# Kernel optimization log

Hardware: AMD Instinct MI355X
Metric: run time of the kernel (lower is better)

The kernel has to match this reference:

```python
import jax, jax.numpy as jnp
import numpy as np

HIDDEN = 4096
INTER = 11008
GROUP = 128
B, S = 1, 2048


def setup_inputs() -> dict:
    key = jax.random.key(0)
    ks = jax.random.split(key, 10)
    inp = {
        "x": jax.random.normal(ks[0], (B, S, HIDDEN), dtype=jnp.float32),
        "gate_qw": jax.random.randint(ks[1], (INTER, HIDDEN), 0, 16, dtype=jnp.int32),
        "gate_qz": jax.random.randint(ks[2], (INTER, HIDDEN // GROUP), 0, 16, dtype=jnp.int32),
        "gate_scale": jax.random.uniform(ks[3], (INTER, HIDDEN // GROUP), dtype=jnp.float32) * 0.02,
        "gate_bias": jnp.zeros((INTER,), dtype=jnp.float32),
        "up_qw": jax.random.randint(ks[4], (INTER, HIDDEN), 0, 16, dtype=jnp.int32),
        "up_qz": jax.random.randint(ks[5], (INTER, HIDDEN // GROUP), 0, 16, dtype=jnp.int32),
        "up_scale": jax.random.uniform(ks[6], (INTER, HIDDEN // GROUP), dtype=jnp.float32) * 0.02,
        "up_bias": jnp.zeros((INTER,), dtype=jnp.float32),
        "down_qw": jax.random.randint(ks[7], (HIDDEN, INTER), 0, 16, dtype=jnp.int32),
        "down_qz": jax.random.randint(ks[8], (HIDDEN, INTER // GROUP), 0, 16, dtype=jnp.int32),
        "down_scale": jax.random.uniform(ks[9], (HIDDEN, INTER // GROUP), dtype=jnp.float32) * 0.02,
        "down_bias": jnp.zeros((HIDDEN,), dtype=jnp.float32),
        "group_size": GROUP,
    }
    return inp


def _dequant(qw, qz, scale, group_size):
    # qw: [O, I] int codes in [0,16); qz, scale: [O, I//g]
    O, I = qw.shape
    g = group_size
    q = qw.reshape(O, I // g, g).astype(jnp.float32)
    w = (q - qz[:, :, None].astype(jnp.float32)) * scale[:, :, None]
    return w.reshape(O, I)  # [O, I]


def reference(x, gate_qw, gate_qz, gate_scale, gate_bias,
              up_qw, up_qz, up_scale, up_bias,
              down_qw, down_qz, down_scale, down_bias, group_size):
    Wg = _dequant(gate_qw, gate_qz, gate_scale, group_size)   # [INTER, HIDDEN]
    Wu = _dequant(up_qw, up_qz, up_scale, group_size)         # [INTER, HIDDEN]
    Wd = _dequant(down_qw, down_qz, down_scale, group_size)   # [HIDDEN, INTER]
    g = jnp.einsum('bsh,ih->bsi', x, Wg) + gate_bias          # [B,S,INTER]
    u = jnp.einsum('bsh,ih->bsi', x, Wu) + up_bias            # [B,S,INTER]
    h = jax.nn.silu(g) * u                                    # SwiGLU
    y = jnp.einsum('bsi,hi->bsh', h, Wd) + down_bias          # [B,S,HIDDEN]
    return y
```

## Files before the change

kernel.cpp:

```cpp
#include <hip/hip_runtime.h>
#include <hip/hip_bf16.h>
#include <stdint.h>

#define SEQ    2048
#define HIDDEN 4096
#define INTER  11008

typedef short bf16x8 __attribute__((ext_vector_type(8)));
typedef float f32x4  __attribute__((ext_vector_type(4)));
typedef unsigned short u16x8 __attribute__((ext_vector_type(8)));

__device__ __forceinline__ unsigned short f2bf(float f) {
    union { __hip_bfloat16 h; unsigned short u; } v;
    v.h = __float2bfloat16(f);
    return v.u;
}

__device__ __forceinline__ void gload_lds16(const void* g, void* lds) {
    __builtin_amdgcn_global_load_lds(
        (const __attribute__((address_space(1))) uint32_t*)g,
        (__attribute__((address_space(3))) uint32_t*)lds,
        16, 0, 0);
}

__device__ __forceinline__ void deq_block(
    const int* __restrict__ qw, const int* __restrict__ qz,
    const float* __restrict__ sc, unsigned short* __restrict__ w,
    int db, int t)
{
    size_t i = (size_t)db * 4096 + (size_t)t * 8;
    int gi = (int)(i >> 7);
    int   z = qz[gi];
    float s = sc[gi];
    float zs = -(float)z * s;
    int4 q0 = *(const int4*)(qw + i);
    int4 q1 = *(const int4*)(qw + i + 4);
    u16x8 o;
    o[0] = f2bf(fmaf((float)q0.x, s, zs));
    o[1] = f2bf(fmaf((float)q0.y, s, zs));
    o[2] = f2bf(fmaf((float)q0.z, s, zs));
    o[3] = f2bf(fmaf((float)q0.w, s, zs));
    o[4] = f2bf(fmaf((float)q1.x, s, zs));
    o[5] = f2bf(fmaf((float)q1.y, s, zs));
    o[6] = f2bf(fmaf((float)q1.z, s, zs));
    o[7] = f2bf(fmaf((float)q1.w, s, zs));
    *(u16x8*)(w + i) = o;
}

__global__ __launch_bounds__(512) void k_prep(
    const float* __restrict__ x, unsigned short* __restrict__ xb,
    const int* __restrict__ gqw, const int* __restrict__ gqz,
    const float* __restrict__ gsc, unsigned short* __restrict__ wgb,
    const int* __restrict__ uqw, const int* __restrict__ uqz,
    const float* __restrict__ usc, unsigned short* __restrict__ wub)
{
    const int bid = blockIdx.x;
    const int t   = threadIdx.x;
    if (bid < 2048) {
        size_t i = ((size_t)bid * 512 + t) * 8;
        float4 v0 = *(const float4*)(x + i);
        float4 v1 = *(const float4*)(x + i + 4);
        u16x8 o;
        o[0] = f2bf(v0.x); o[1] = f2bf(v0.y); o[2] = f2bf(v0.z); o[3] = f2bf(v0.w);
        o[4] = f2bf(v1.x); o[5] = f2bf(v1.y); o[6] = f2bf(v1.z); o[7] = f2bf(v1.w);
        *(u16x8*)(xb + i) = o;
    } else if (bid < 13056) {
        deq_block(gqw, gqz, gsc, wgb, bid - 2048, t);
    } else {
        deq_block(uqw, uqz, usc, wub, bid - 13056, t);
    }
}

__global__ __launch_bounds__(512) void k_deq_fb(
    const int* __restrict__ qw, const int* __restrict__ qz,
    const float* __restrict__ sc, unsigned short* __restrict__ w)
{
    deq_block(qw, qz, sc, w, blockIdx.x, threadIdx.x);
}

__global__ __launch_bounds__(512) void k_gate_up(
    const unsigned short* __restrict__ xb,
    const unsigned short* __restrict__ wg,
    const unsigned short* __restrict__ wu,
    const float* __restrict__ gbias, const float* __restrict__ ubias,
    unsigned short* __restrict__ h,
    const int* __restrict__ dqw, const int* __restrict__ dqz,
    const float* __restrict__ dsc, unsigned short* __restrict__ wdb)
{
    __shared__ __align__(16) unsigned short At[128 * 64];
    __shared__ __align__(16) unsigned short Bg[128 * 64];
    __shared__ __align__(16) unsigned short Bu[128 * 64];

    if (blockIdx.x >= 1376) {
        deq_block(dqw, dqz, dsc, wdb, blockIdx.x - 1376, threadIdx.x);
        return;
    }

    const int orig = blockIdx.x;
    const int swz  = (orig & 7) * 172 + (orig >> 3);
    const int mt   = swz & 15;
    const int nt   = swz >> 4;
    const int m0   = mt * 128;
    const int n0   = nt * 128;

    const int t    = threadIdx.x;
    const int lane = t & 63;
    const int wave = t >> 6;
    const int wm = (wave >> 2) * 64;
    const int wn = (wave & 3) * 32;

    f32x4 accG[4][2], accU[4][2];
#pragma unroll
    for (int mi = 0; mi < 4; ++mi)
#pragma unroll
        for (int ni = 0; ni < 2; ++ni) {
            accG[mi][ni] = (f32x4){0.f, 0.f, 0.f, 0.f};
            accU[mi][ni] = (f32x4){0.f, 0.f, 0.f, 0.f};
        }

    for (int kt = 0; kt < HIDDEN / 64; ++kt) {
        const int k0 = kt * 64;

#pragma unroll
        for (int cc = 0; cc < 2; ++cc) {
            int idx  = t + 512 * cc;
            int row  = idx >> 3;
            int scol = ((idx & 7) * 16) ^ ((row & 7) << 4);
            gload_lds16((const char*)(xb + (size_t)(m0 + row) * HIDDEN + k0) + scol,
                        (char*)At + idx * 16);
            gload_lds16((const char*)(wg + (size_t)(n0 + row) * HIDDEN + k0) + scol,
                        (char*)Bg + idx * 16);
            gload_lds16((const char*)(wu + (size_t)(n0 + row) * HIDDEN + k0) + scol,
                        (char*)Bu + idx * 16);
        }

        __syncthreads();

#pragma unroll
        for (int kk = 0; kk < 2; ++kk) {
            bf16x8 af[4], bg[2], bu[2];
#pragma unroll
            for (int mi = 0; mi < 4; ++mi) {
                int row  = wm + mi * 16 + (lane & 15);
                int colb = kk * 64 + ((lane >> 4) * 16);
                af[mi] = *(const bf16x8*)((const char*)At + row * 128 +
                                          (colb ^ ((row & 7) << 4)));
            }
#pragma unroll
            for (int ni = 0; ni < 2; ++ni) {
                int row  = wn + ni * 16 + (lane & 15);
                int colb = kk * 64 + ((lane >> 4) * 16);
                int off  = row * 128 + (colb ^ ((row & 7) << 4));
                bg[ni] = *(const bf16x8*)((const char*)Bg + off);
                bu[ni] = *(const bf16x8*)((const char*)Bu + off);
            }
            __builtin_amdgcn_s_setprio(1);
#pragma unroll
            for (int mi = 0; mi < 4; ++mi)
#pragma unroll
                for (int ni = 0; ni < 2; ++ni) {
                    accG[mi][ni] = __builtin_amdgcn_mfma_f32_16x16x32_bf16(
                        af[mi], bg[ni], accG[mi][ni], 0, 0, 0);
                    accU[mi][ni] = __builtin_amdgcn_mfma_f32_16x16x32_bf16(
                        af[mi], bu[ni], accU[mi][ni], 0, 0, 0);
                }
            __builtin_amdgcn_s_setprio(0);
        }

        __syncthreads();
    }

#pragma unroll
    for (int ni = 0; ni < 2; ++ni) {
        int col = n0 + wn + ni * 16 + (lane & 15);
        float gb = gbias[col], ub = ubias[col];
#pragma unroll
        for (int mi = 0; mi < 4; ++mi) {
#pragma unroll
            for (int j = 0; j < 4; ++j) {
                int row = m0 + wm + mi * 16 + ((lane >> 4) * 4) + j;
                float g = accG[mi][ni][j] + gb;
                float u = accU[mi][ni][j] + ub;
                float sig = 1.f / (1.f + __expf(-g));
                h[(size_t)row * INTER + col] = f2bf(g * sig * u);
            }
        }
    }
}

__global__ __launch_bounds__(512) void k_down(
    const unsigned short* __restrict__ h,
    const unsigned short* __restrict__ wd,
    const float* __restrict__ dbias,
    float* __restrict__ y)
{
    __shared__ __align__(16) unsigned short At[128 * 64];
    __shared__ __align__(16) unsigned short Bd[128 * 64];

    const int orig = blockIdx.x;
    const int swz  = (orig & 7) * 64 + (orig >> 3);
    const int mt   = swz & 15;
    const int nt   = swz >> 4;
    const int m0   = mt * 128;
    const int n0   = nt * 128;

    const int t    = threadIdx.x;
    const int lane = t & 63;
    const int wave = t >> 6;
    const int wm = (wave >> 2) * 64;
    const int wn = (wave & 3) * 32;

    f32x4 acc[4][2];
#pragma unroll
    for (int mi = 0; mi < 4; ++mi)
#pragma unroll
        for (int ni = 0; ni < 2; ++ni)
            acc[mi][ni] = (f32x4){0.f, 0.f, 0.f, 0.f};

    for (int kt = 0; kt < INTER / 64; ++kt) {
        const int k0 = kt * 64;

#pragma unroll
        for (int cc = 0; cc < 2; ++cc) {
            int idx  = t + 512 * cc;
            int row  = idx >> 3;
            int scol = ((idx & 7) * 16) ^ ((row & 7) << 4);
            gload_lds16((const char*)(h + (size_t)(m0 + row) * INTER + k0) + scol,
                        (char*)At + idx * 16);
            gload_lds16((const char*)(wd + (size_t)(n0 + row) * INTER + k0) + scol,
                        (char*)Bd + idx * 16);
        }

        __syncthreads();

#pragma unroll
        for (int kk = 0; kk < 2; ++kk) {
            bf16x8 af[4], bd[2];
#pragma unroll
            for (int mi = 0; mi < 4; ++mi) {
                int row  = wm + mi * 16 + (lane & 15);
                int colb = kk * 64 + ((lane >> 4) * 16);
                af[mi] = *(const bf16x8*)((const char*)At + row * 128 +
                                          (colb ^ ((row & 7) << 4)));
            }
#pragma unroll
            for (int ni = 0; ni < 2; ++ni) {
                int row  = wn + ni * 16 + (lane & 15);
                int colb = kk * 64 + ((lane >> 4) * 16);
                bd[ni] = *(const bf16x8*)((const char*)Bd + row * 128 +
                                          (colb ^ ((row & 7) << 4)));
            }
            __builtin_amdgcn_s_setprio(1);
#pragma unroll
            for (int mi = 0; mi < 4; ++mi)
#pragma unroll
                for (int ni = 0; ni < 2; ++ni)
                    acc[mi][ni] = __builtin_amdgcn_mfma_f32_16x16x32_bf16(
                        af[mi], bd[ni], acc[mi][ni], 0, 0, 0);
            __builtin_amdgcn_s_setprio(0);
        }

        __syncthreads();
    }

#pragma unroll
    for (int ni = 0; ni < 2; ++ni) {
        int col = n0 + wn + ni * 16 + (lane & 15);
        float db = dbias[col];
#pragma unroll
        for (int mi = 0; mi < 4; ++mi) {
#pragma unroll
            for (int j = 0; j < 4; ++j) {
                int row = m0 + wm + mi * 16 + ((lane >> 4) * 4) + j;
                y[(size_t)row * HIDDEN + col] = acc[mi][ni][j] + db;
            }
        }
    }
}

extern "C" void kernel_launch(void* const* d_in, const int* in_sizes, int n_in,
                              void* d_out, int out_size, void* d_ws, size_t ws_size,
                              hipStream_t stream) {
    const float* x    = (const float*)d_in[0];
    const int*   gqw  = (const int*)d_in[1];
    const int*   gqz  = (const int*)d_in[2];
    const float* gsc  = (const float*)d_in[3];
    const float* gbia = (const float*)d_in[4];
    const int*   uqw  = (const int*)d_in[5];
    const int*   uqz  = (const int*)d_in[6];
    const float* usc  = (const float*)d_in[7];
    const float* ubia = (const float*)d_in[8];
    const int*   dqw  = (const int*)d_in[9];
    const int*   dqz  = (const int*)d_in[10];
    const float* dsc  = (const float*)d_in[11];
    const float* dbia = (const float*)d_in[12];
    float* y = (float*)d_out;

    const size_t N_XB = (size_t)SEQ * HIDDEN;
    const size_t N_H  = (size_t)SEQ * INTER;
    const size_t N_W  = (size_t)INTER * HIDDEN;

    unsigned short* xb  = (unsigned short*)d_ws;
    unsigned short* hh  = xb + N_XB;
    unsigned short* wgb = hh + N_H;
    unsigned short* wub = wgb + N_W;

    const size_t need_big = (N_XB + N_H + 3 * N_W) * sizeof(unsigned short);
    const bool   big      = ws_size >= need_big;

    k_prep<<<dim3(24064), 512, 0, stream>>>(x, xb, gqw, gqz, gsc, wgb,
                                            uqw, uqz, usc, wub);

    if (big) {
        unsigned short* wdb = wub + N_W;
        k_gate_up<<<dim3(1376 + 11008), 512, 0, stream>>>(
            xb, wgb, wub, gbia, ubia, hh, dqw, dqz, dsc, wdb);
        k_down<<<dim3(512), 512, 0, stream>>>(hh, wdb, dbia, y);
    } else {
        unsigned short* wdb = wgb;
        k_gate_up<<<dim3(1376), 512, 0, stream>>>(
            xb, wgb, wub, gbia, ubia, hh, dqw, dqz, dsc, wdb);
        k_deq_fb<<<dim3(11008), 512, 0, stream>>>(dqw, dqz, dsc, wdb);
        k_down<<<dim3(512), 512, 0, stream>>>(hh, wdb, dbia, y);
    }
}
```

Baseline: 700.8 us.

## Switch gate/up GEMM to int8 MFMA with per-row activation quantization

```diff
diff --git a/kernel.cpp b/kernel.cpp
--- a/kernel.cpp
+++ b/kernel.cpp
@@ -8,6 +8,9 @@
 
 typedef short bf16x8 __attribute__((ext_vector_type(8)));
 typedef float f32x4  __attribute__((ext_vector_type(4)));
+typedef float f32x16 __attribute__((ext_vector_type(16)));
+typedef int   i32x4  __attribute__((ext_vector_type(4)));
+typedef int   i32x16 __attribute__((ext_vector_type(16)));
 typedef unsigned short u16x8 __attribute__((ext_vector_type(8)));
 
 __device__ __forceinline__ unsigned short f2bf(float f) {
@@ -23,12 +26,62 @@
         16, 0, 0);
 }
 
-__device__ __forceinline__ void deq_block(
+__global__ __launch_bounds__(512) void k_prep(
+    const float* __restrict__ x, signed char* __restrict__ xq,
+    float* __restrict__ ax,
+    const int* __restrict__ gqw, const int* __restrict__ gqz,
+    signed char* __restrict__ wg8,
+    const int* __restrict__ uqw, const int* __restrict__ uqz,
+    signed char* __restrict__ wu8)
+{
+    const int bid = blockIdx.x;
+    const int t   = threadIdx.x;
+    if (bid < 2048) {
+        __shared__ float wmx[8];
+        const float* xr = x + (size_t)bid * HIDDEN + t * 8;
+        float v[8]; float m = 0.f;
+#pragma unroll
+        for (int j = 0; j < 8; ++j) { v[j] = xr[j]; m = fmaxf(m, fabsf(v[j])); }
+#pragma unroll
+        for (int off = 32; off; off >>= 1) m = fmaxf(m, __shfl_xor(m, off));
+        if ((t & 63) == 0) wmx[t >> 6] = m;
+        __syncthreads();
+        m = wmx[0];
+#pragma unroll
+        for (int w = 1; w < 8; ++w) m = fmaxf(m, wmx[w]);
+        float inv = m > 0.f ? 127.f / m : 0.f;
+        int q[8];
+#pragma unroll
+        for (int j = 0; j < 8; ++j) {
+            int qi = (int)rintf(v[j] * inv);
+            q[j] = qi < -127 ? -127 : (qi > 127 ? 127 : qi);
+        }
+        int w0 = (q[0]&255) | ((q[1]&255)<<8) | ((q[2]&255)<<16) | ((q[3]&255)<<24);
+        int w1 = (q[4]&255) | ((q[5]&255)<<8) | ((q[6]&255)<<16) | ((q[7]&255)<<24);
+        ((int2*)(xq + (size_t)bid * HIDDEN))[t] = make_int2(w0, w1);
+        if (t == 0) ax[bid] = m / 127.f;
+    } else {
+        const int* qw; const int* qz; signed char* w8; int row;
+        if (bid < 13056) { qw = gqw; qz = gqz; w8 = wg8; row = bid - 2048; }
+        else             { qw = uqw; qz = uqz; w8 = wu8; row = bid - 13056; }
+        size_t base = (size_t)row * HIDDEN + t * 8;
+        int4 q0 = *(const int4*)(qw + base);
+        int4 q1 = *(const int4*)(qw + base + 4);
+        int z = qz[row * (HIDDEN / 128) + (t >> 4)];
+        int w0 = ((q0.x-z)&255) | (((q0.y-z)&255)<<8) |
+                 (((q0.z-z)&255)<<16) | (((q0.w-z)&255)<<24);
+        int w1 = ((q1.x-z)&255) | (((q1.y-z)&255)<<8) |
+                 (((q1.z-z)&255)<<16) | (((q1.w-z)&255)<<24);
+        ((int2*)(w8 + (size_t)row * HIDDEN))[t] = make_int2(w0, w1);
+    }
+}
+
+__device__ __forceinline__ void deq_block256(
     const int* __restrict__ qw, const int* __restrict__ qz,
     const float* __restrict__ sc, unsigned short* __restrict__ w,
     int db, int t)
 {
-    size_t i = (size_t)db * 4096 + (size_t)t * 8;
+    size_t i = (size_t)db * 2048 + (size_t)t * 8;
     int gi = (int)(i >> 7);
     int   z = qz[gi];
     float s = sc[gi];
@@ -47,143 +100,121 @@
     *(u16x8*)(w + i) = o;
 }
 
-__global__ __launch_bounds__(512) void k_prep(
-    const float* __restrict__ x, unsigned short* __restrict__ xb,
-    const int* __restrict__ gqw, const int* __restrict__ gqz,
-    const float* __restrict__ gsc, unsigned short* __restrict__ wgb,
-    const int* __restrict__ uqw, const int* __restrict__ uqz,
-    const float* __restrict__ usc, unsigned short* __restrict__ wub)
-{
-    const int bid = blockIdx.x;
-    const int t   = threadIdx.x;
-    if (bid < 2048) {
-        size_t i = ((size_t)bid * 512 + t) * 8;
-        float4 v0 = *(const float4*)(x + i);
-        float4 v1 = *(const float4*)(x + i + 4);
-        u16x8 o;
-        o[0] = f2bf(v0.x); o[1] = f2bf(v0.y); o[2] = f2bf(v0.z); o[3] = f2bf(v0.w);
-        o[4] = f2bf(v1.x); o[5] = f2bf(v1.y); o[6] = f2bf(v1.z); o[7] = f2bf(v1.w);
-        *(u16x8*)(xb + i) = o;
-    } else if (bid < 13056) {
-        deq_block(gqw, gqz, gsc, wgb, bid - 2048, t);
-    } else {
-        deq_block(uqw, uqz, usc, wub, bid - 13056, t);
-    }
-}
-
-__global__ __launch_bounds__(512) void k_deq_fb(
-    const int* __restrict__ qw, const int* __restrict__ qz,
-    const float* __restrict__ sc, unsigned short* __restrict__ w)
-{
-    deq_block(qw, qz, sc, w, blockIdx.x, threadIdx.x);
-}
-
-__global__ __launch_bounds__(512) void k_gate_up(
-    const unsigned short* __restrict__ xb,
-    const unsigned short* __restrict__ wg,
-    const unsigned short* __restrict__ wu,
+__global__ __launch_bounds__(256, 2) void k_gate_up_i8(
+    const signed char* __restrict__ xq, const float* __restrict__ ax,
+    const signed char* __restrict__ wg8, const signed char* __restrict__ wu8,
+    const float* __restrict__ gsc, const float* __restrict__ usc,
     const float* __restrict__ gbias, const float* __restrict__ ubias,
     unsigned short* __restrict__ h,
     const int* __restrict__ dqw, const int* __restrict__ dqz,
     const float* __restrict__ dsc, unsigned short* __restrict__ wdb)
 {
-    __shared__ __align__(16) unsigned short At[128 * 64];
-    __shared__ __align__(16) unsigned short Bg[128 * 64];
-    __shared__ __align__(16) unsigned short Bu[128 * 64];
-
-    if (blockIdx.x >= 1376) {
-        deq_block(dqw, dqz, dsc, wdb, blockIdx.x - 1376, threadIdx.x);
+    __shared__ __align__(16) signed char At[128 * 128];
+    __shared__ __align__(16) signed char Bg[64 * 128];
+    __shared__ __align__(16) signed char Bu[64 * 128];
+
+    if (blockIdx.x >= 2752) {
+        deq_block256(dqw, dqz, dsc, wdb, blockIdx.x - 2752, threadIdx.x);
         return;
     }
 
     const int orig = blockIdx.x;
-    const int swz  = (orig & 7) * 172 + (orig >> 3);
+    const int swz  = (orig & 7) * 344 + (orig >> 3);
     const int mt   = swz & 15;
     const int nt   = swz >> 4;
     const int m0   = mt * 128;
-    const int n0   = nt * 128;
-
-    const int t    = threadIdx.x;
-    const int lane = t & 63;
-    const int wave = t >> 6;
-    const int wm = (wave >> 2) * 64;
-    const int wn = (wave & 3) * 32;
-
-    f32x4 accG[4][2], accU[4][2];
-#pragma unroll
-    for (int mi = 0; mi < 4; ++mi)
-#pragma unroll
-        for (int ni = 0; ni < 2; ++ni) {
-            accG[mi][ni] = (f32x4){0.f, 0.f, 0.f, 0.f};
-            accU[mi][ni] = (f32x4){0.f, 0.f, 0.f, 0.f};
-        }
-
-    for (int kt = 0; kt < HIDDEN / 64; ++kt) {
-        const int k0 = kt * 64;
-
+    const int n0   = nt * 64;
+
+    const int t     = threadIdx.x;
+    const int lane  = t & 63;
+    const int wave  = t >> 6;
+    const int wm    = (wave >> 1) * 64;
+    const int wn    = (wave & 1) * 32;
+    const int lrow  = lane & 31;
+    const int khalf = lane >> 5;
+    const int col   = n0 + wn + lrow;
+
+    f32x16 gF[2], uF[2];
+#pragma unroll
+    for (int mi = 0; mi < 2; ++mi)
+#pragma unroll
+        for (int j = 0; j < 16; ++j) { gF[mi][j] = 0.f; uF[mi][j] = 0.f; }
+
+    for (int kt = 0; kt < HIDDEN / 128; ++kt) {
+        const int k0 = kt * 128;
+
+#pragma unroll
+        for (int cc = 0; cc < 4; ++cc) {
+            int idx = t + 256 * cc;
+            int row = idx >> 3, sl = idx & 7;
+            gload_lds16(xq + (size_t)(m0 + row) * HIDDEN + k0 + ((sl ^ (row & 7)) * 16),
+                        (char*)At + idx * 16);
+        }
 #pragma unroll
         for (int cc = 0; cc < 2; ++cc) {
-            int idx  = t + 512 * cc;
-            int row  = idx >> 3;
-            int scol = ((idx & 7) * 16) ^ ((row & 7) << 4);
-            gload_lds16((const char*)(xb + (size_t)(m0 + row) * HIDDEN + k0) + scol,
-                        (char*)At + idx * 16);
-            gload_lds16((const char*)(wg + (size_t)(n0 + row) * HIDDEN + k0) + scol,
-                        (char*)Bg + idx * 16);
-            gload_lds16((const char*)(wu + (size_t)(n0 + row) * HIDDEN + k0) + scol,
-                        (char*)Bu + idx * 16);
-        }
-
-        __syncthreads();
-
-#pragma unroll
-        for (int kk = 0; kk < 2; ++kk) {
-            bf16x8 af[4], bg[2], bu[2];
-#pragma unroll
-            for (int mi = 0; mi < 4; ++mi) {
-                int row  = wm + mi * 16 + (lane & 15);
-                int colb = kk * 64 + ((lane >> 4) * 16);
-                af[mi] = *(const bf16x8*)((const char*)At + row * 128 +
-                                          (colb ^ ((row & 7) << 4)));
-            }
-#pragma unroll
-            for (int ni = 0; ni < 2; ++ni) {
-                int row  = wn + ni * 16 + (lane & 15);
-                int colb = kk * 64 + ((lane >> 4) * 16);
-                int off  = row * 128 + (colb ^ ((row & 7) << 4));
-                bg[ni] = *(const bf16x8*)((const char*)Bg + off);
-                bu[ni] = *(const bf16x8*)((const char*)Bu + off);
-            }
+            int idx = t + 256 * cc;
+            int row = idx >> 3, sl = idx & 7;
+            int go  = (sl ^ (row & 7)) * 16;
+            gload_lds16(wg8 + (size_t)(n0 + row) * HIDDEN + k0 + go, (char*)Bg + idx * 16);
+            gload_lds16(wu8 + (size_t)(n0 + row) * HIDDEN + k0 + go, (char*)Bu + idx * 16);
+        }
+
+        __syncthreads();
+
+        float sg = gsc[(size_t)col * (HIDDEN / 128) + kt];
+        float su = usc[(size_t)col * (HIDDEN / 128) + kt];
+
+        i32x16 gI[2], uI[2];
+#pragma unroll
+        for (int ks = 0; ks < 4; ++ks) {
+            int slot = 2 * ks + khalf;
+            int r0 = wm + lrow;
+            int r1 = wm + 32 + lrow;
+            int rb = wn + lrow;
+            i32x4 a0  = *(const i32x4*)(At + r0 * 128 + ((slot ^ (r0 & 7)) * 16));
+            i32x4 a1  = *(const i32x4*)(At + r1 * 128 + ((slot ^ (r1 & 7)) * 16));
+            i32x4 bgv = *(const i32x4*)(Bg + rb * 128 + ((slot ^ (rb & 7)) * 16));
+            i32x4 buv = *(const i32x4*)(Bu + rb * 128 + ((slot ^ (rb & 7)) * 16));
             __builtin_amdgcn_s_setprio(1);
-#pragma unroll
-            for (int mi = 0; mi < 4; ++mi)
-#pragma unroll
-                for (int ni = 0; ni < 2; ++ni) {
-                    accG[mi][ni] = __builtin_amdgcn_mfma_f32_16x16x32_bf16(
-                        af[mi], bg[ni], accG[mi][ni], 0, 0, 0);
-                    accU[mi][ni] = __builtin_amdgcn_mfma_f32_16x16x32_bf16(
-                        af[mi], bu[ni], accU[mi][ni], 0, 0, 0);
-                }
+            if (ks == 0) {
+                i32x16 z16;
+#pragma unroll
+                for (int j = 0; j < 16; ++j) z16[j] = 0;
+                gI[0] = __builtin_amdgcn_mfma_i32_32x32x32_i8(a0, bgv, z16, 0, 0, 0);
+                gI[1] = __builtin_amdgcn_mfma_i32_32x32x32_i8(a1, bgv, z16, 0, 0, 0);
+                uI[0] = __builtin_amdgcn_mfma_i32_32x32x32_i8(a0, buv, z16, 0, 0, 0);
+                uI[1] = __builtin_amdgcn_mfma_i32_32x32x32_i8(a1, buv, z16, 0, 0, 0);
+            } else {
+                gI[0] = __builtin_amdgcn_mfma_i32_32x32x32_i8(a0, bgv, gI[0], 0, 0, 0);
+                gI[1] = __builtin_amdgcn_mfma_i32_32x32x32_i8(a1, bgv, gI[1], 0, 0, 0);
+                uI[0] = __builtin_amdgcn_mfma_i32_32x32x32_i8(a0, buv, uI[0], 0, 0, 0);
+                uI[1] = __builtin_amdgcn_mfma_i32_32x32x32_i8(a1, buv, uI[1], 0, 0, 0);
+            }
             __builtin_amdgcn_s_setprio(0);
         }
 
         __syncthreads();
-    }
-
-#pragma unroll
-    for (int ni = 0; ni < 2; ++ni) {
-        int col = n0 + wn + ni * 16 + (lane & 15);
-        float gb = gbias[col], ub = ubias[col];
-#pragma unroll
-        for (int mi = 0; mi < 4; ++mi) {
-#pragma unroll
-            for (int j = 0; j < 4; ++j) {
-                int row = m0 + wm + mi * 16 + ((lane >> 4) * 4) + j;
-                float g = accG[mi][ni][j] + gb;
-                float u = accU[mi][ni][j] + ub;
-                float sig = 1.f / (1.f + __expf(-g));
-                h[(size_t)row * INTER + col] = f2bf(g * sig * u);
-            }
+
+#pragma unroll
+        for (int mi = 0; mi < 2; ++mi)
+#pragma unroll
+            for (int j = 0; j < 16; ++j) {
+                gF[mi][j] = fmaf((float)gI[mi][j], sg, gF[mi][j]);
+                uF[mi][j] = fmaf((float)uI[mi][j], su, uF[mi][j]);
+            }
+    }
+
+    float gb = gbias[col], ub = ubias[col];
+#pragma unroll
+    for (int mi = 0; mi < 2; ++mi) {
+#pragma unroll
+        for (int j = 0; j < 16; ++j) {
+            int row = m0 + wm + mi * 32 + (j & 3) + 8 * (j >> 2) + 4 * khalf;
+            float axv = ax[row];
+            float g = gF[mi][j] * axv + gb;
+            float u = uF[mi][j] * axv + ub;
+            float sig = 1.f / (1.f + __expf(-g));
+            h[(size_t)row * INTER + col] = f2bf(g * sig * u);
         }
     }
 }
@@ -296,31 +327,17 @@
     const float* dbia = (const float*)d_in[12];
     float* y = (float*)d_out;
 
-    const size_t N_XB = (size_t)SEQ * HIDDEN;
-    const size_t N_H  = (size_t)SEQ * INTER;
-    const size_t N_W  = (size_t)INTER * HIDDEN;
-
-    unsigned short* xb  = (unsigned short*)d_ws;
-    unsigned short* hh  = xb + N_XB;
-    unsigned short* wgb = hh + N_H;
-    unsigned short* wub = wgb + N_W;
-
-    const size_t need_big = (N_XB + N_H + 3 * N_W) * sizeof(unsigned short);
-    const bool   big      = ws_size >= need_big;
-
-    k_prep<<<dim3(24064), 512, 0, stream>>>(x, xb, gqw, gqz, gsc, wgb,
-                                            uqw, uqz, usc, wub);
-
-    if (big) {
-        unsigned short* wdb = wub + N_W;
-        k_gate_up<<<dim3(1376 + 11008), 512, 0, stream>>>(
-            xb, wgb, wub, gbia, ubia, hh, dqw, dqz, dsc, wdb);
-        k_down<<<dim3(512), 512, 0, stream>>>(hh, wdb, dbia, y);
-    } else {
-        unsigned short* wdb = wgb;
-        k_gate_up<<<dim3(1376), 512, 0, stream>>>(
-            xb, wgb, wub, gbia, ubia, hh, dqw, dqz, dsc, wdb);
-        k_deq_fb<<<dim3(11008), 512, 0, stream>>>(dqw, dqz, dsc, wdb);
-        k_down<<<dim3(512), 512, 0, stream>>>(hh, wdb, dbia, y);
-    }
-}
+    char* p = (char*)d_ws;
+    signed char* xq = (signed char*)p;        p += (size_t)SEQ * HIDDEN;
+    float* ax       = (float*)p;              p += (size_t)SEQ * 4;
+    signed char* wg8 = (signed char*)p;       p += (size_t)INTER * HIDDEN;
+    signed char* wu8 = (signed char*)p;       p += (size_t)INTER * HIDDEN;
+    unsigned short* hh  = (unsigned short*)p; p += (size_t)SEQ * INTER * 2;
+    unsigned short* wdb = (unsigned short*)p;
+
+    k_prep<<<dim3(24064), 512, 0, stream>>>(x, xq, ax, gqw, gqz, wg8,
+                                            uqw, uqz, wu8);
+    k_gate_up_i8<<<dim3(2752 + 22016), 256, 0, stream>>>(
+        xq, ax, wg8, wu8, gsc, usc, gbia, ubia, hh, dqw, dqz, dsc, wdb);
+    k_down<<<dim3(512), 512, 0, stream>>>(hh, wdb, dbia, y);
+}
```

Measured after the change: 686.9 us. 2.0% less time.

## Triple-buffer LDS tiles with staggered async prefetch in gate/up and down GEMMs

Applied to the files above, without the earlier changes.

```diff
diff --git a/kernel.cpp b/kernel.cpp
--- a/kernel.cpp
+++ b/kernel.cpp
@@ -9,6 +9,11 @@
 typedef short bf16x8 __attribute__((ext_vector_type(8)));
 typedef float f32x4  __attribute__((ext_vector_type(4)));
 typedef unsigned short u16x8 __attribute__((ext_vector_type(8)));
+
+#define BAR()  asm volatile("s_barrier" ::: "memory")
+#define W6()   asm volatile("s_waitcnt vmcnt(6)" ::: "memory")
+#define W4()   asm volatile("s_waitcnt vmcnt(4)" ::: "memory")
+#define W0()   asm volatile("s_waitcnt vmcnt(0)" ::: "memory")
 
 __device__ __forceinline__ unsigned short f2bf(float f) {
     union { __hip_bfloat16 h; unsigned short u; } v;
@@ -87,9 +92,9 @@
     const int* __restrict__ dqw, const int* __restrict__ dqz,
     const float* __restrict__ dsc, unsigned short* __restrict__ wdb)
 {
-    __shared__ __align__(16) unsigned short At[128 * 64];
-    __shared__ __align__(16) unsigned short Bg[128 * 64];
-    __shared__ __align__(16) unsigned short Bu[128 * 64];
+    __shared__ __align__(16) unsigned short A_[3][128 * 64];
+    __shared__ __align__(16) unsigned short Bg_[3][128 * 64];
+    __shared__ __align__(16) unsigned short Bu_[3][128 * 64];
 
     if (blockIdx.x >= 1376) {
         deq_block(dqw, dqz, dsc, wdb, blockIdx.x - 1376, threadIdx.x);
@@ -97,9 +102,9 @@
     }
 
     const int orig = blockIdx.x;
-    const int swz  = (orig & 7) * 172 + (orig >> 3);
-    const int mt   = swz & 15;
-    const int nt   = swz >> 4;
+    const int swzb = (orig & 7) * 172 + (orig >> 3);
+    const int mt   = swzb & 15;
+    const int nt   = swzb >> 4;
     const int m0   = mt * 128;
     const int n0   = nt * 128;
 
@@ -118,56 +123,135 @@
             accU[mi][ni] = (f32x4){0.f, 0.f, 0.f, 0.f};
         }
 
-    for (int kt = 0; kt < HIDDEN / 64; ++kt) {
+    auto stA = [&](int buf, int kt) {
         const int k0 = kt * 64;
-
 #pragma unroll
         for (int cc = 0; cc < 2; ++cc) {
             int idx  = t + 512 * cc;
             int row  = idx >> 3;
             int scol = ((idx & 7) * 16) ^ ((row & 7) << 4);
             gload_lds16((const char*)(xb + (size_t)(m0 + row) * HIDDEN + k0) + scol,
-                        (char*)At + idx * 16);
+                        (char*)A_[buf] + idx * 16);
+        }
+    };
+    auto stG = [&](int buf, int kt) {
+        const int k0 = kt * 64;
+#pragma unroll
+        for (int cc = 0; cc < 2; ++cc) {
+            int idx  = t + 512 * cc;
+            int row  = idx >> 3;
+            int scol = ((idx & 7) * 16) ^ ((row & 7) << 4);
             gload_lds16((const char*)(wg + (size_t)(n0 + row) * HIDDEN + k0) + scol,
-                        (char*)Bg + idx * 16);
+                        (char*)Bg_[buf] + idx * 16);
+        }
+    };
+    auto stU = [&](int buf, int kt) {
+        const int k0 = kt * 64;
+#pragma unroll
+        for (int cc = 0; cc < 2; ++cc) {
+            int idx  = t + 512 * cc;
+            int row  = idx >> 3;
+            int scol = ((idx & 7) * 16) ^ ((row & 7) << 4);
             gload_lds16((const char*)(wu + (size_t)(n0 + row) * HIDDEN + k0) + scol,
-                        (char*)Bu + idx * 16);
-        }
-
-        __syncthreads();
-
-#pragma unroll
-        for (int kk = 0; kk < 2; ++kk) {
-            bf16x8 af[4], bg[2], bu[2];
-#pragma unroll
-            for (int mi = 0; mi < 4; ++mi) {
-                int row  = wm + mi * 16 + (lane & 15);
-                int colb = kk * 64 + ((lane >> 4) * 16);
-                af[mi] = *(const bf16x8*)((const char*)At + row * 128 +
-                                          (colb ^ ((row & 7) << 4)));
-            }
-#pragma unroll
-            for (int ni = 0; ni < 2; ++ni) {
-                int row  = wn + ni * 16 + (lane & 15);
-                int colb = kk * 64 + ((lane >> 4) * 16);
-                int off  = row * 128 + (colb ^ ((row & 7) << 4));
-                bg[ni] = *(const bf16x8*)((const char*)Bg + off);
-                bu[ni] = *(const bf16x8*)((const char*)Bu + off);
-            }
-            __builtin_amdgcn_s_setprio(1);
-#pragma unroll
-            for (int mi = 0; mi < 4; ++mi)
-#pragma unroll
-                for (int ni = 0; ni < 2; ++ni) {
-                    accG[mi][ni] = __builtin_amdgcn_mfma_f32_16x16x32_bf16(
-                        af[mi], bg[ni], accG[mi][ni], 0, 0, 0);
-                    accU[mi][ni] = __builtin_amdgcn_mfma_f32_16x16x32_bf16(
-                        af[mi], bu[ni], accU[mi][ni], 0, 0, 0);
-                }
-            __builtin_amdgcn_s_setprio(0);
-        }
-
-        __syncthreads();
+                        (char*)Bu_[buf] + idx * 16);
+        }
+    };
+
+    stA(0, 0); stG(0, 0); stU(0, 0);
+    stA(1, 1); stG(1, 1); stU(1, 1);
+    W6(); BAR();
+
+    for (int kt = 0; kt < 64; ++kt) {
+        const int cur = kt % 3;
+        const int nxt = (kt + 2) % 3;
+        const bool pf = (kt + 2) < 64;
+        bf16x8 af[4], bb[2];
+
+        if (pf) stA(nxt, kt + 2);
+#pragma unroll
+        for (int mi = 0; mi < 4; ++mi) {
+            int row  = wm + mi * 16 + (lane & 15);
+            int colb = (lane >> 4) * 16;
+            af[mi] = *(const bf16x8*)((const char*)A_[cur] + row * 128 +
+                                      (colb ^ ((row & 7) << 4)));
+        }
+#pragma unroll
+        for (int ni = 0; ni < 2; ++ni) {
+            int row  = wn + ni * 16 + (lane & 15);
+            int colb = (lane >> 4) * 16;
+            bb[ni] = *(const bf16x8*)((const char*)Bg_[cur] + row * 128 +
+                                      (colb ^ ((row & 7) << 4)));
+        }
+        __builtin_amdgcn_s_setprio(1);
+#pragma unroll
+        for (int mi = 0; mi < 4; ++mi)
+#pragma unroll
+            for (int ni = 0; ni < 2; ++ni)
+                accG[mi][ni] = __builtin_amdgcn_mfma_f32_16x16x32_bf16(
+                    af[mi], bb[ni], accG[mi][ni], 0, 0, 0);
+        __builtin_amdgcn_s_setprio(0);
+        BAR();
+
+        if (pf) stG(nxt, kt + 2);
+#pragma unroll
+        for (int ni = 0; ni < 2; ++ni) {
+            int row  = wn + ni * 16 + (lane & 15);
+            int colb = (lane >> 4) * 16;
+            bb[ni] = *(const bf16x8*)((const char*)Bu_[cur] + row * 128 +
+                                      (colb ^ ((row & 7) << 4)));
+        }
+        __builtin_amdgcn_s_setprio(1);
+#pragma unroll
+        for (int mi = 0; mi < 4; ++mi)
+#pragma unroll
+            for (int ni = 0; ni < 2; ++ni)
+                accU[mi][ni] = __builtin_amdgcn_mfma_f32_16x16x32_bf16(
+                    af[mi], bb[ni], accU[mi][ni], 0, 0, 0);
+        __builtin_amdgcn_s_setprio(0);
+        BAR();
+
+        if (pf) stU(nxt, kt + 2);
+#pragma unroll
+        for (int mi = 0; mi < 4; ++mi) {
+            int row  = wm + mi * 16 + (lane & 15);
+            int colb = 64 + (lane >> 4) * 16;
+            af[mi] = *(const bf16x8*)((const char*)A_[cur] + row * 128 +
+                                      (colb ^ ((row & 7) << 4)));
+        }
+#pragma unroll
+        for (int ni = 0; ni < 2; ++ni) {
+            int row  = wn + ni * 16 + (lane & 15);
+            int colb = 64 + (lane >> 4) * 16;
+            bb[ni] = *(const bf16x8*)((const char*)Bg_[cur] + row * 128 +
+                                      (colb ^ ((row & 7) << 4)));
+        }
+        __builtin_amdgcn_s_setprio(1);
+#pragma unroll
+        for (int mi = 0; mi < 4; ++mi)
+#pragma unroll
+            for (int ni = 0; ni < 2; ++ni)
+                accG[mi][ni] = __builtin_amdgcn_mfma_f32_16x16x32_bf16(
+                    af[mi], bb[ni], accG[mi][ni], 0, 0, 0);
+        __builtin_amdgcn_s_setprio(0);
+        BAR();
+
+#pragma unroll
+        for (int ni = 0; ni < 2; ++ni) {
+            int row  = wn + ni * 16 + (lane & 15);
+            int colb = 64 + (lane >> 4) * 16;
+            bb[ni] = *(const bf16x8*)((const char*)Bu_[cur] + row * 128 +
+                                      (colb ^ ((row & 7) << 4)));
+        }
+        __builtin_amdgcn_s_setprio(1);
+#pragma unroll
+        for (int mi = 0; mi < 4; ++mi)
+#pragma unroll
+            for (int ni = 0; ni < 2; ++ni)
+                accU[mi][ni] = __builtin_amdgcn_mfma_f32_16x16x32_bf16(
+                    af[mi], bb[ni], accU[mi][ni], 0, 0, 0);
+        __builtin_amdgcn_s_setprio(0);
+        if (kt < 62)       { W6(); BAR(); }
+        else if (kt == 62) { W0(); BAR(); }
     }
 
 #pragma unroll
@@ -194,13 +278,13 @@
     const float* __restrict__ dbias,
     float* __restrict__ y)
 {
-    __shared__ __align__(16) unsigned short At[128 * 64];
-    __shared__ __align__(16) unsigned short Bd[128 * 64];
+    __shared__ __align__(16) unsigned short A_[3][128 * 64];
+    __shared__ __align__(16) unsigned short B_[3][128 * 64];
 
     const int orig = blockIdx.x;
-    const int swz  = (orig & 7) * 64 + (orig >> 3);
-    const int mt   = swz & 15;
-    const int nt   = swz >> 4;
+    const int swzb = (orig & 7) * 64 + (orig >> 3);
+    const int mt   = swzb & 15;
+    const int nt   = swzb >> 4;
     const int m0   = mt * 128;
     const int n0   = nt * 128;
 
@@ -217,50 +301,89 @@
         for (int ni = 0; ni < 2; ++ni)
             acc[mi][ni] = (f32x4){0.f, 0.f, 0.f, 0.f};
 
-    for (int kt = 0; kt < INTER / 64; ++kt) {
+    auto stA = [&](int buf, int kt) {
         const int k0 = kt * 64;
-
 #pragma unroll
         for (int cc = 0; cc < 2; ++cc) {
             int idx  = t + 512 * cc;
             int row  = idx >> 3;
             int scol = ((idx & 7) * 16) ^ ((row & 7) << 4);
             gload_lds16((const char*)(h + (size_t)(m0 + row) * INTER + k0) + scol,
-                        (char*)At + idx * 16);
+                        (char*)A_[buf] + idx * 16);
+        }
+    };
+    auto stB = [&](int buf, int kt) {
+        const int k0 = kt * 64;
+#pragma unroll
+        for (int cc = 0; cc < 2; ++cc) {
+            int idx  = t + 512 * cc;
+            int row  = idx >> 3;
+            int scol = ((idx & 7) * 16) ^ ((row & 7) << 4);
             gload_lds16((const char*)(wd + (size_t)(n0 + row) * INTER + k0) + scol,
-                        (char*)Bd + idx * 16);
-        }
-
-        __syncthreads();
-
-#pragma unroll
-        for (int kk = 0; kk < 2; ++kk) {
-            bf16x8 af[4], bd[2];
-#pragma unroll
-            for (int mi = 0; mi < 4; ++mi) {
-                int row  = wm + mi * 16 + (lane & 15);
-                int colb = kk * 64 + ((lane >> 4) * 16);
-                af[mi] = *(const bf16x8*)((const char*)At + row * 128 +
-                                          (colb ^ ((row & 7) << 4)));
-            }
-#pragma unroll
-            for (int ni = 0; ni < 2; ++ni) {
-                int row  = wn + ni * 16 + (lane & 15);
-                int colb = kk * 64 + ((lane >> 4) * 16);
-                bd[ni] = *(const bf16x8*)((const char*)Bd + row * 128 +
-                                          (colb ^ ((row & 7) << 4)));
-            }
-            __builtin_amdgcn_s_setprio(1);
-#pragma unroll
-            for (int mi = 0; mi < 4; ++mi)
-#pragma unroll
-                for (int ni = 0; ni < 2; ++ni)
-                    acc[mi][ni] = __builtin_amdgcn_mfma_f32_16x16x32_bf16(
-                        af[mi], bd[ni], acc[mi][ni], 0, 0, 0);
-            __builtin_amdgcn_s_setprio(0);
-        }
-
-        __syncthreads();
+                        (char*)B_[buf] + idx * 16);
+        }
+    };
+
+    stA(0, 0); stB(0, 0);
+    stA(1, 1); stB(1, 1);
+    W4(); BAR();
+
+    for (int kt = 0; kt < 172; ++kt) {
+        const int cur = kt % 3;
+        const int nxt = (kt + 2) % 3;
+        const bool pf = (kt + 2) < 172;
+        bf16x8 af[4], bd[2];
+
+        if (pf) stA(nxt, kt + 2);
+#pragma unroll
+        for (int mi = 0; mi < 4; ++mi) {
+            int row  = wm + mi * 16 + (lane & 15);
+            int colb = (lane >> 4) * 16;
+            af[mi] = *(const bf16x8*)((const char*)A_[cur] + row * 128 +
+                                      (colb ^ ((row & 7) << 4)));
+        }
+#pragma unroll
+        for (int ni = 0; ni < 2; ++ni) {
+            int row  = wn + ni * 16 + (lane & 15);
+            int colb = (lane >> 4) * 16;
+            bd[ni] = *(const bf16x8*)((const char*)B_[cur] + row * 128 +
+                                      (colb ^ ((row & 7) << 4)));
+        }
+        __builtin_amdgcn_s_setprio(1);
+#pragma unroll
+        for (int mi = 0; mi < 4; ++mi)
+#pragma unroll
+            for (int ni = 0; ni < 2; ++ni)
+                acc[mi][ni] = __builtin_amdgcn_mfma_f32_16x16x32_bf16(
+                    af[mi], bd[ni], acc[mi][ni], 0, 0, 0);
+        __builtin_amdgcn_s_setprio(0);
+        BAR();
+
+        if (pf) stB(nxt, kt + 2);
+#pragma unroll
+        for (int mi = 0; mi < 4; ++mi) {
+            int row  = wm + mi * 16 + (lane & 15);
+            int colb = 64 + (lane >> 4) * 16;
+            af[mi] = *(const bf16x8*)((const char*)A_[cur] + row * 128 +
+                                      (colb ^ ((row & 7) << 4)));
+        }
+#pragma unroll
+        for (int ni = 0; ni < 2; ++ni) {
+            int row  = wn + ni * 16 + (lane & 15);
+            int colb = 64 + (lane >> 4) * 16;
+            bd[ni] = *(const bf16x8*)((const char*)B_[cur] + row * 128 +
+                                      (colb ^ ((row & 7) << 4)));
+        }
+        __builtin_amdgcn_s_setprio(1);
+#pragma unroll
+        for (int mi = 0; mi < 4; ++mi)
+#pragma unroll
+            for (int ni = 0; ni < 2; ++ni)
+                acc[mi][ni] = __builtin_amdgcn_mfma_f32_16x16x32_bf16(
+                    af[mi], bd[ni], acc[mi][ni], 0, 0, 0);
+        __builtin_amdgcn_s_setprio(0);
+        if (kt < 170)       { W4(); BAR(); }
+        else if (kt == 170) { W0(); BAR(); }
     }
 
 #pragma unroll
```

Result: slower. 1.329 ms (+89.6%).

## Enlarge gate/up tile to 256x128 with double-buffered LDS pipeline

Applied to the files above, without the earlier changes.

```diff
diff --git a/kernel.cpp b/kernel.cpp
--- a/kernel.cpp
+++ b/kernel.cpp
@@ -9,6 +9,11 @@
 typedef short bf16x8 __attribute__((ext_vector_type(8)));
 typedef float f32x4  __attribute__((ext_vector_type(4)));
 typedef unsigned short u16x8 __attribute__((ext_vector_type(8)));
+
+#define BAR()  asm volatile("s_barrier" ::: "memory")
+#define W4()   asm volatile("s_waitcnt vmcnt(4)" ::: "memory")
+#define W2()   asm volatile("s_waitcnt vmcnt(2)" ::: "memory")
+#define W0()   asm volatile("s_waitcnt vmcnt(0)" ::: "memory")
 
 __device__ __forceinline__ unsigned short f2bf(float f) {
     union { __hip_bfloat16 h; unsigned short u; } v;
@@ -87,91 +92,147 @@
     const int* __restrict__ dqw, const int* __restrict__ dqz,
     const float* __restrict__ dsc, unsigned short* __restrict__ wdb)
 {
-    __shared__ __align__(16) unsigned short At[128 * 64];
-    __shared__ __align__(16) unsigned short Bg[128 * 64];
-    __shared__ __align__(16) unsigned short Bu[128 * 64];
-
-    if (blockIdx.x >= 1376) {
-        deq_block(dqw, dqz, dsc, wdb, blockIdx.x - 1376, threadIdx.x);
+    __shared__ __align__(16) unsigned short A_[2][256 * 64];
+    __shared__ __align__(16) unsigned short Bg_[2][128 * 64];
+    __shared__ __align__(16) unsigned short Bu_[2][128 * 64];
+
+    if (blockIdx.x >= 688) {
+        deq_block(dqw, dqz, dsc, wdb, blockIdx.x - 688, threadIdx.x);
         return;
     }
 
     const int orig = blockIdx.x;
-    const int swz  = (orig & 7) * 172 + (orig >> 3);
-    const int mt   = swz & 15;
-    const int nt   = swz >> 4;
-    const int m0   = mt * 128;
+    const int swz  = (orig & 7) * 86 + (orig >> 3);
+    const int mt   = swz & 7;
+    const int nt   = swz >> 3;
+    const int m0   = mt * 256;
     const int n0   = nt * 128;
 
     const int t    = threadIdx.x;
     const int lane = t & 63;
     const int wave = t >> 6;
-    const int wm = (wave >> 2) * 64;
-    const int wn = (wave & 3) * 32;
-
-    f32x4 accG[4][2], accU[4][2];
+    const int wm = (wave >> 1) * 64;
+    const int wn = (wave & 1) * 64;
+
+    f32x4 accG[4][4], accU[4][4];
 #pragma unroll
     for (int mi = 0; mi < 4; ++mi)
 #pragma unroll
-        for (int ni = 0; ni < 2; ++ni) {
+        for (int ni = 0; ni < 4; ++ni) {
             accG[mi][ni] = (f32x4){0.f, 0.f, 0.f, 0.f};
             accU[mi][ni] = (f32x4){0.f, 0.f, 0.f, 0.f};
         }
 
-    for (int kt = 0; kt < HIDDEN / 64; ++kt) {
-        const int k0 = kt * 64;
-
+    auto stA0 = [&](int buf, int kt) {
+        const int k0 = kt * 64;
 #pragma unroll
         for (int cc = 0; cc < 2; ++cc) {
             int idx  = t + 512 * cc;
             int row  = idx >> 3;
             int scol = ((idx & 7) * 16) ^ ((row & 7) << 4);
             gload_lds16((const char*)(xb + (size_t)(m0 + row) * HIDDEN + k0) + scol,
-                        (char*)At + idx * 16);
+                        (char*)A_[buf] + idx * 16);
+        }
+    };
+    auto stA1 = [&](int buf, int kt) {
+        const int k0 = kt * 64;
+#pragma unroll
+        for (int cc = 0; cc < 2; ++cc) {
+            int idx  = t + 512 * cc;
+            int row  = idx >> 3;
+            int scol = ((idx & 7) * 16) ^ ((row & 7) << 4);
+            gload_lds16((const char*)(xb + (size_t)(m0 + 128 + row) * HIDDEN + k0) + scol,
+                        (char*)A_[buf] + 16384 + idx * 16);
+        }
+    };
+    auto stG = [&](int buf, int kt) {
+        const int k0 = kt * 64;
+#pragma unroll
+        for (int cc = 0; cc < 2; ++cc) {
+            int idx  = t + 512 * cc;
+            int row  = idx >> 3;
+            int scol = ((idx & 7) * 16) ^ ((row & 7) << 4);
             gload_lds16((const char*)(wg + (size_t)(n0 + row) * HIDDEN + k0) + scol,
-                        (char*)Bg + idx * 16);
+                        (char*)Bg_[buf] + idx * 16);
+        }
+    };
+    auto stU = [&](int buf, int kt) {
+        const int k0 = kt * 64;
+#pragma unroll
+        for (int cc = 0; cc < 2; ++cc) {
+            int idx  = t + 512 * cc;
+            int row  = idx >> 3;
+            int scol = ((idx & 7) * 16) ^ ((row & 7) << 4);
             gload_lds16((const char*)(wu + (size_t)(n0 + row) * HIDDEN + k0) + scol,
-                        (char*)Bu + idx * 16);
-        }
-
-        __syncthreads();
-
-#pragma unroll
-        for (int kk = 0; kk < 2; ++kk) {
-            bf16x8 af[4], bg[2], bu[2];
-#pragma unroll
-            for (int mi = 0; mi < 4; ++mi) {
-                int row  = wm + mi * 16 + (lane & 15);
-                int colb = kk * 64 + ((lane >> 4) * 16);
-                af[mi] = *(const bf16x8*)((const char*)At + row * 128 +
-                                          (colb ^ ((row & 7) << 4)));
-            }
-#pragma unroll
-            for (int ni = 0; ni < 2; ++ni) {
-                int row  = wn + ni * 16 + (lane & 15);
-                int colb = kk * 64 + ((lane >> 4) * 16);
-                int off  = row * 128 + (colb ^ ((row & 7) << 4));
-                bg[ni] = *(const bf16x8*)((const char*)Bg + off);
-                bu[ni] = *(const bf16x8*)((const char*)Bu + off);
-            }
-            __builtin_amdgcn_s_setprio(1);
-#pragma unroll
-            for (int mi = 0; mi < 4; ++mi)
-#pragma unroll
-                for (int ni = 0; ni < 2; ++ni) {
-                    accG[mi][ni] = __builtin_amdgcn_mfma_f32_16x16x32_bf16(
-                        af[mi], bg[ni], accG[mi][ni], 0, 0, 0);
-                    accU[mi][ni] = __builtin_amdgcn_mfma_f32_16x16x32_bf16(
-                        af[mi], bu[ni], accU[mi][ni], 0, 0, 0);
-                }
-            __builtin_amdgcn_s_setprio(0);
-        }
-
-        __syncthreads();
-    }
-
-#pragma unroll
-    for (int ni = 0; ni < 2; ++ni) {
+                        (char*)Bu_[buf] + idx * 16);
+        }
+    };
+
+    auto rdA = [&](int buf, int kk, bf16x8* af) {
+#pragma unroll
+        for (int mi = 0; mi < 4; ++mi) {
+            int row  = wm + mi * 16 + (lane & 15);
+            int colb = kk * 64 + ((lane >> 4) * 16);
+            af[mi] = *(const bf16x8*)((const char*)A_[buf] + row * 128 +
+                                      (colb ^ ((row & 7) << 4)));
+        }
+    };
+    auto rdB = [&](const unsigned short* Bt, int kk, bf16x8* bb) {
+#pragma unroll
+        for (int ni = 0; ni < 4; ++ni) {
+            int row  = wn + ni * 16 + (lane & 15);
+            int colb = kk * 64 + ((lane >> 4) * 16);
+            bb[ni] = *(const bf16x8*)((const char*)Bt + row * 128 +
+                                      (colb ^ ((row & 7) << 4)));
+        }
+    };
+    auto mmG = [&](const bf16x8* af, const bf16x8* bb) {
+        __builtin_amdgcn_s_setprio(1);
+#pragma unroll
+        for (int mi = 0; mi < 4; ++mi)
+#pragma unroll
+            for (int ni = 0; ni < 4; ++ni)
+                accG[mi][ni] = __builtin_amdgcn_mfma_f32_16x16x32_bf16(
+                    af[mi], bb[ni], accG[mi][ni], 0, 0, 0);
+        __builtin_amdgcn_s_setprio(0);
+    };
+    auto mmU = [&](const bf16x8* af, const bf16x8* bb) {
+        __builtin_amdgcn_s_setprio(1);
+#pragma unroll
+        for (int mi = 0; mi < 4; ++mi)
+#pragma unroll
+            for (int ni = 0; ni < 4; ++ni)
+                accU[mi][ni] = __builtin_amdgcn_mfma_f32_16x16x32_bf16(
+                    af[mi], bb[ni], accU[mi][ni], 0, 0, 0);
+        __builtin_amdgcn_s_setprio(0);
+    };
+
+    stA0(0, 0); stA1(0, 0); stG(0, 0); stU(0, 0);
+
+    for (int kt = 0; kt < 63; ++kt) {
+        const int b = kt & 1;
+        bf16x8 af[4], bb[4];
+        stA0(b ^ 1, kt + 1); W4(); BAR();
+        rdA(b, 0, af); rdB(Bg_[b], 0, bb); mmG(af, bb); BAR();
+        stA1(b ^ 1, kt + 1); W4(); BAR();
+        rdB(Bu_[b], 0, bb); mmU(af, bb); BAR();
+        stG(b ^ 1, kt + 1); BAR();
+        rdA(b, 1, af); rdB(Bg_[b], 1, bb); mmG(af, bb); BAR();
+        stU(b ^ 1, kt + 1); BAR();
+        rdB(Bu_[b], 1, bb); mmU(af, bb); BAR();
+    }
+    {
+        bf16x8 af[4], bb[4];
+        W2(); BAR();
+        rdA(1, 0, af); rdB(Bg_[1], 0, bb); mmG(af, bb); BAR();
+        W0(); BAR();
+        rdB(Bu_[1], 0, bb); mmU(af, bb); BAR();
+        rdA(1, 1, af); rdB(Bg_[1], 1, bb); mmG(af, bb); BAR();
+        rdB(Bu_[1], 1, bb); mmU(af, bb);
+    }
+
+#pragma unroll
+    for (int ni = 0; ni < 4; ++ni) {
         int col = n0 + wn + ni * 16 + (lane & 15);
         float gb = gbias[col], ub = ubias[col];
 #pragma unroll
@@ -313,12 +374,12 @@
 
     if (big) {
         unsigned short* wdb = wub + N_W;
-        k_gate_up<<<dim3(1376 + 11008), 512, 0, stream>>>(
+        k_gate_up<<<dim3(688 + 11008), 512, 0, stream>>>(
             xb, wgb, wub, gbia, ubia, hh, dqw, dqz, dsc, wdb);
         k_down<<<dim3(512), 512, 0, stream>>>(hh, wdb, dbia, y);
     } else {
         unsigned short* wdb = wgb;
-        k_gate_up<<<dim3(1376), 512, 0, stream>>>(
+        k_gate_up<<<dim3(688), 512, 0, stream>>>(
             xb, wgb, wub, gbia, ubia, hh, dqw, dqz, dsc, wdb);
         k_deq_fb<<<dim3(11008), 512, 0, stream>>>(dqw, dqz, dsc, wdb);
         k_down<<<dim3(512), 512, 0, stream>>>(hh, wdb, dbia, y);
```

Measured after the change: 891.6 us. 1.27x slower.
